# Kernel optimization log

Measured on AMD Instinct MI355X. Metric: run time of the kernel, lower is better.

## Reference

```python
import jax, jax.numpy as jnp
import numpy as np

B, I, H, R = 8192, 512, 1024, 64  # batch, input_size, hidden_size, rank (w_rank == u_ranks[-1])


def setup_inputs() -> dict:
    key = jax.random.key(0)
    ks = jax.random.split(key, 11)
    f = jax.random.normal
    return {
        "x": f(ks[0], (B, I), jnp.float32),
        "h": f(ks[1], (B, H), jnp.float32),
        "c": f(ks[2], (B, H), jnp.float32),
        "u_x": 0.1 * f(ks[3], (I, R), jnp.float32),
        "u_h": 0.1 * f(ks[4], (H, R), jnp.float32),
        "v_x": 0.1 * f(ks[5], (4 * H, R), jnp.float32),
        "v_h": 0.1 * f(ks[6], (4 * H, R), jnp.float32),
        "b_x": 0.1 * f(ks[7], (4 * H,), jnp.float32),
        "b_h": 0.1 * f(ks[8], (4 * H,), jnp.float32),
        "dia_x": 0.1 * f(ks[9], (1, I), jnp.float32),
        "dia_h": 0.1 * f(ks[10], (1, H), jnp.float32),
    }


def reference(x, h, c, u_x, u_h, v_x, v_h, b_x, b_h, dia_x, dia_h):
    Bn = x.shape[0]
    # diagonal (vector-multiplication) terms; vm_x padded to hidden size (H >= I)
    vm_x = jnp.pad(dia_x * x, ((0, 0), (0, H - I)))          # [B, H]
    vm_h = dia_h * h                                          # [B, H]
    # low-rank projections: [B,R] @ [R,4H]
    lowered_x = (x @ u_x) @ v_x.T                             # [B, 4H]
    lowered_h = (h @ u_h) @ v_h.T                             # [B, 4H]
    # vectorized form of the 4-gate refinement loop
    v_x4 = v_x.reshape(4, H, R)
    v_h4 = v_h.reshape(4, H, R)
    coef_x = jnp.sum(u_x[None] * v_x4[:, :I, :], axis=-1)    # [4, I]
    coef_h = jnp.sum(u_h[None] * v_h4, axis=-1)              # [4, H]
    ref_x = jnp.pad(x[:, None, :] * coef_x[None], ((0, 0), (0, 0), (0, H - I))).reshape(Bn, 4 * H)
    ref_h = (h[:, None, :] * coef_h[None]).reshape(Bn, 4 * H)
    gx = lowered_x - ref_x + b_x
    gh = lowered_h - ref_h + b_h
    xi, xf, xo, xn = jnp.split(gx, 4, axis=1)
    hi, hf, ho, hn = jnp.split(gh, 4, axis=1)
    z = vm_x + vm_h
    inputgate = jax.nn.sigmoid(xi + hi + z)
    forgetgate = jax.nn.sigmoid(xf + hf + z)
    outputgate = jax.nn.sigmoid(xo + ho + z)
    newgate = jnp.tanh(xn + hn + z)
    c_next = forgetgate * c + inputgate * newgate
    h_next = outputgate * jnp.tanh(c_next)
    return h_next, c_next
```

## Files before the change

kernel.cpp:

```cpp
#include <hip/hip_runtime.h>
#include <hip/hip_bf16.h>

#define B_ 8192
#define I_ 512
#define H_ 1024
#define R_ 64

typedef __bf16 bf16x8 __attribute__((ext_vector_type(8)));
typedef short  s16x8  __attribute__((ext_vector_type(8)));
typedef float  f32x4  __attribute__((ext_vector_type(4)));

static __device__ __forceinline__ short f2bf(float f) {
    union { float f; unsigned u; } v; v.f = f;
    unsigned r = v.u + 0x7fffu + ((v.u >> 16) & 1u);
    return (short)(r >> 16);
}
static __device__ __forceinline__ float frcp_(float x) {
#if __has_builtin(__builtin_amdgcn_rcpf)
    return __builtin_amdgcn_rcpf(x);
#else
    float r; asm("v_rcp_f32 %0, %1" : "=v"(r) : "v"(x)); return r;
#endif
}
static __device__ __forceinline__ float sigmoidf_(float v) {
    return frcp_(1.f + __expf(-v));
}
static __device__ __forceinline__ float tanhf_(float v) {
    return 2.f * frcp_(1.f + __expf(-2.f * v)) - 1.f;
}

__global__ __launch_bounds__(256) void prep_kernel(
    const float* __restrict__ u_x, const float* __restrict__ u_h,
    const float* __restrict__ v_x, const float* __restrict__ v_h,
    short* __restrict__ uxT, short* __restrict__ uhT, short* __restrict__ Vc,
    float* __restrict__ coef_x, float* __restrict__ coef_h)
{
    int t = blockIdx.x * 256 + threadIdx.x;
    if (t < 64 * 512) {
        int k = t >> 6, r = t & 63;
        uxT[r * 512 + k] = f2bf(u_x[t]);
        return;
    }
    t -= 64 * 512;
    if (t < 64 * 1024) {
        int k = t >> 6, r = t & 63;
        uhT[r * 1024 + k] = f2bf(u_h[t]);
        return;
    }
    t -= 64 * 1024;
    if (t < 4096 * 128) {
        int n = t >> 7, q = t & 127;
        Vc[t] = f2bf(q < 64 ? v_x[n * 64 + q] : v_h[n * 64 + (q - 64)]);
        return;
    }
    t -= 4096 * 128;
    if (t < 1536 * 64) {
        const int wid = t >> 6, lane = t & 63;
        const float* U; const float* V; float* C; int j, JN;
        if (wid < 512) { U = u_x; V = v_x; C = coef_x; j = wid;       JN = 512;  }
        else           { U = u_h; V = v_h; C = coef_h; j = wid - 512; JN = 1024; }
        const float uv = U[(size_t)j * 64 + lane];
        float s[4];
#pragma unroll
        for (int g = 0; g < 4; ++g)
            s[g] = uv * V[(size_t)(g * H_ + j) * 64 + lane];
#pragma unroll
        for (int off = 32; off >= 1; off >>= 1)
#pragma unroll
            for (int g = 0; g < 4; ++g)
                s[g] += __shfl_xor(s[g], off, 64);
        if (lane == 0)
#pragma unroll
            for (int g = 0; g < 4; ++g)
                C[g * JN + j] = s[g];
        return;
    }
}

__global__ __launch_bounds__(256) void stage1_kernel(
    const float* __restrict__ x, const float* __restrict__ h,
    const short* __restrict__ uxT, const short* __restrict__ uhT,
    short* __restrict__ P)
{
    __shared__ short At[16 * 136];
    const int w = threadIdx.x >> 6, lane = threadIdx.x & 63;
    const int quad = lane >> 4, lr = lane & 15;
    const int n0 = w * 16;

    const float* X; const short* UT; int K, co;
    if (blockIdx.y == 0) { X = x; UT = uxT; K = I_; co = 0; }
    else                 { X = h; UT = uhT; K = H_; co = 64; }

    const int b0 = blockIdx.x * 16;
    const int srow = threadIdx.x >> 4;
    const int scol = (threadIdx.x & 15) * 8;

    f32x4 acc = {};
    const short* bp = UT + (size_t)(n0 + lr) * K + quad * 8;
    const short* arow = At + lr * 136 + quad * 8;
    const float* srcbase = X + (size_t)(b0 + srow) * K + scol;

    float4 c0 = ((const float4*)(srcbase))[0];
    float4 c1 = ((const float4*)(srcbase))[1];

    for (int k0 = 0; k0 < K; k0 += 128) {
        s16x8 p;
        p[0] = f2bf(c0.x); p[1] = f2bf(c0.y); p[2] = f2bf(c0.z); p[3] = f2bf(c0.w);
        p[4] = f2bf(c1.x); p[5] = f2bf(c1.y); p[6] = f2bf(c1.z); p[7] = f2bf(c1.w);
        __syncthreads();
        *(s16x8*)(At + srow * 136 + scol) = p;
        __syncthreads();
        if (k0 + 128 < K) {
            c0 = ((const float4*)(srcbase + k0 + 128))[0];
            c1 = ((const float4*)(srcbase + k0 + 128))[1];
        }
#pragma unroll
        for (int ks = 0; ks < 4; ++ks) {
            bf16x8 bfrag = *(const bf16x8*)(bp + k0 + ks * 32);
            bf16x8 afrag = *(const bf16x8*)(arow + ks * 32);
            acc = __builtin_amdgcn_mfma_f32_16x16x32_bf16(afrag, bfrag, acc, 0, 0, 0);
        }
    }

#pragma unroll
    for (int r = 0; r < 4; ++r)
        P[(size_t)(b0 + quad * 4 + r) * 128 + co + n0 + lr] = f2bf(acc[r]);
}

__global__ __launch_bounds__(256) void stage2_kernel(
    const short* __restrict__ P, const short* __restrict__ Vc,
    const float* __restrict__ x, const float* __restrict__ h,
    const float* __restrict__ c,
    const float* __restrict__ coef_x, const float* __restrict__ coef_h,
    const float* __restrict__ b_x, const float* __restrict__ b_h,
    const float* __restrict__ dia_x, const float* __restrict__ dia_h,
    float* __restrict__ out)
{
    const int lane = threadIdx.x & 63;
    const int wv   = threadIdx.x >> 6;
    const int quad = lane >> 4, lr = lane & 15;
    const int b0 = blockIdx.x * 64;
    const int j0 = blockIdx.y * 64 + wv * 16;
    const int j = j0 + lr;
    const bool jx = (j < I_);

    bf16x8 bfr[4][4];
#pragma unroll
    for (int g = 0; g < 4; ++g)
#pragma unroll
        for (int ks = 0; ks < 4; ++ks)
            bfr[g][ks] = *(const bf16x8*)(Vc + (size_t)(g * H_ + j0 + lr) * 128 + ks * 32 + quad * 8);

    const float dx = jx ? dia_x[j] : 0.f;
    const float dh = dia_h[j];
    float cx[4], ch[4], bsum[4];
#pragma unroll
    for (int g = 0; g < 4; ++g) {
        cx[g]   = jx ? coef_x[g * I_ + j] : 0.f;
        ch[g]   = coef_h[g * H_ + j];
        bsum[g] = b_x[g * H_ + j] + b_h[g * H_ + j];
    }

    bf16x8 a[4];
#pragma unroll
    for (int ks = 0; ks < 4; ++ks)
        a[ks] = *(const bf16x8*)(P + (size_t)(b0 + lr) * 128 + ks * 32 + quad * 8);
    float xv[4], hv[4], cv[4];
#pragma unroll
    for (int r = 0; r < 4; ++r) {
        const int brow = b0 + quad * 4 + r;
        cv[r] = c[(size_t)brow * H_ + j];
        hv[r] = h[(size_t)brow * H_ + j];
        xv[r] = jx ? x[(size_t)brow * I_ + j] : 0.f;
    }

    for (int mt = 0; mt < 4; ++mt) {
        bf16x8 an[4];
        float xn[4], hn[4], cn2[4];
        if (mt < 3) {
            const int rb = b0 + (mt + 1) * 16;
#pragma unroll
            for (int ks = 0; ks < 4; ++ks)
                an[ks] = *(const bf16x8*)(P + (size_t)(rb + lr) * 128 + ks * 32 + quad * 8);
#pragma unroll
            for (int r = 0; r < 4; ++r) {
                const int brow = rb + quad * 4 + r;
                cn2[r] = c[(size_t)brow * H_ + j];
                hn[r]  = h[(size_t)brow * H_ + j];
                xn[r]  = jx ? x[(size_t)brow * I_ + j] : 0.f;
            }
        }

        f32x4 acc[4] = {};
#pragma unroll
        for (int ks = 0; ks < 4; ++ks)
#pragma unroll
            for (int g = 0; g < 4; ++g)
                acc[g] = __builtin_amdgcn_mfma_f32_16x16x32_bf16(a[ks], bfr[g][ks], acc[g], 0, 0, 0);

#pragma unroll
        for (int r = 0; r < 4; ++r) {
            const int brow = b0 + mt * 16 + quad * 4 + r;
            const float xe = xv[r], he = hv[r];
            const float z  = dx * xe + dh * he;

            const float g0 = acc[0][r] - xe * cx[0] - he * ch[0] + bsum[0] + z;
            const float g1 = acc[1][r] - xe * cx[1] - he * ch[1] + bsum[1] + z;
            const float g2 = acc[2][r] - xe * cx[2] - he * ch[2] + bsum[2] + z;
            const float g3 = acc[3][r] - xe * cx[3] - he * ch[3] + bsum[3] + z;

            const float ig = sigmoidf_(g0);
            const float fg = sigmoidf_(g1);
            const float og = sigmoidf_(g2);
            const float ng = tanhf_(g3);

            const float cn = fg * cv[r] + ig * ng;
            const float hnv = og * tanhf_(cn);

            out[(size_t)brow * H_ + j] = hnv;
            out[(size_t)B_ * H_ + (size_t)brow * H_ + j] = cn;
        }

        if (mt < 3) {
#pragma unroll
            for (int ks = 0; ks < 4; ++ks) a[ks] = an[ks];
#pragma unroll
            for (int r = 0; r < 4; ++r) { xv[r] = xn[r]; hv[r] = hn[r]; cv[r] = cn2[r]; }
        }
    }
}

extern "C" void kernel_launch(void* const* d_in, const int* in_sizes, int n_in,
                              void* d_out, int out_size, void* d_ws, size_t ws_size,
                              hipStream_t stream) {
    const float* x     = (const float*)d_in[0];
    const float* h     = (const float*)d_in[1];
    const float* c     = (const float*)d_in[2];
    const float* u_x   = (const float*)d_in[3];
    const float* u_h   = (const float*)d_in[4];
    const float* v_x   = (const float*)d_in[5];
    const float* v_h   = (const float*)d_in[6];
    const float* b_x   = (const float*)d_in[7];
    const float* b_h   = (const float*)d_in[8];
    const float* dia_x = (const float*)d_in[9];
    const float* dia_h = (const float*)d_in[10];
    float* out = (float*)d_out;

    char* ws = (char*)d_ws;
    short* P      = (short*)(ws);
    short* uxT    = (short*)(ws + 2097152);
    short* uhT    = (short*)(ws + 2097152 + 65536);
    short* Vc     = (short*)(ws + 2097152 + 65536 + 131072);
    float* coef_x = (float*)(ws + 2097152 + 65536 + 131072 + 1048576);
    float* coef_h = (float*)(ws + 2097152 + 65536 + 131072 + 1048576 + 8192);

    prep_kernel<<<2816, 256, 0, stream>>>(u_x, u_h, v_x, v_h, uxT, uhT, Vc, coef_x, coef_h);
    stage1_kernel<<<dim3(512, 2), 256, 0, stream>>>(x, h, uxT, uhT, P);
    stage2_kernel<<<dim3(128, 16), 256, 0, stream>>>(P, Vc, x, h, c,
                                                     coef_x, coef_h, b_x, b_h,
                                                     dia_x, dia_h, out);
}
```

Before: 194.8 us.

## Swap MFMA operands so each lane owns 4 contiguous hidden columns for vector I/O

The MFMA operand order in stage2 is swapped (V fragment as A, P as B), so the output tile is transposed and each lane holds four consecutive hidden columns of one batch row. This allows 16-byte vector loads of x/h/c and the per-column parameters, and 16-byte nontemporal stores of h_next and c_next, replacing scalar strided accesses. It raises register use for the per-lane 4x4 parameter arrays, and the jx check now uses the warp's column base j0, which relies on I being a multiple of 16.

```diff
diff --git a/kernel.cpp b/kernel.cpp
--- a/kernel.cpp
+++ b/kernel.cpp
@@ -141,91 +141,98 @@
     const int quad = lane >> 4, lr = lane & 15;
     const int b0 = blockIdx.x * 64;
     const int j0 = blockIdx.y * 64 + wv * 16;
-    const int j = j0 + lr;
-    const bool jx = (j < I_);
-
-    bf16x8 bfr[4][4];
-#pragma unroll
-    for (int g = 0; g < 4; ++g)
-#pragma unroll
-        for (int ks = 0; ks < 4; ++ks)
-            bfr[g][ks] = *(const bf16x8*)(Vc + (size_t)(g * H_ + j0 + lr) * 128 + ks * 32 + quad * 8);
-
-    const float dx = jx ? dia_x[j] : 0.f;
-    const float dh = dia_h[j];
-    float cx[4], ch[4], bsum[4];
-#pragma unroll
-    for (int g = 0; g < 4; ++g) {
-        cx[g]   = jx ? coef_x[g * I_ + j] : 0.f;
-        ch[g]   = coef_h[g * H_ + j];
-        bsum[g] = b_x[g * H_ + j] + b_h[g * H_ + j];
-    }
+    const int j4 = j0 + quad * 4;
+    const bool jx = (j0 < I_);
 
     bf16x8 a[4];
 #pragma unroll
     for (int ks = 0; ks < 4; ++ks)
         a[ks] = *(const bf16x8*)(P + (size_t)(b0 + lr) * 128 + ks * 32 + quad * 8);
-    float xv[4], hv[4], cv[4];
-#pragma unroll
-    for (int r = 0; r < 4; ++r) {
-        const int brow = b0 + quad * 4 + r;
-        cv[r] = c[(size_t)brow * H_ + j];
-        hv[r] = h[(size_t)brow * H_ + j];
-        xv[r] = jx ? x[(size_t)brow * I_ + j] : 0.f;
+    f32x4 xv = {}, hv, cv;
+    {
+        const int brow = b0 + lr;
+        cv = *(const f32x4*)(c + (size_t)brow * H_ + j4);
+        hv = *(const f32x4*)(h + (size_t)brow * H_ + j4);
+        if (jx) xv = *(const f32x4*)(x + (size_t)brow * I_ + j4);
+    }
+
+    bf16x8 vfr[4][4];
+#pragma unroll
+    for (int g = 0; g < 4; ++g)
+#pragma unroll
+        for (int ks = 0; ks < 4; ++ks)
+            vfr[g][ks] = *(const bf16x8*)(Vc + (size_t)(g * H_ + j0 + lr) * 128 + ks * 32 + quad * 8);
+
+    float dx[4] = {}, dh[4], cx[4][4] = {}, ch[4][4], bs[4][4];
+    {
+        f32x4 t;
+        if (jx) { t = *(const f32x4*)(dia_x + j4); dx[0]=t[0]; dx[1]=t[1]; dx[2]=t[2]; dx[3]=t[3]; }
+        t = *(const f32x4*)(dia_h + j4); dh[0]=t[0]; dh[1]=t[1]; dh[2]=t[2]; dh[3]=t[3];
+#pragma unroll
+        for (int g = 0; g < 4; ++g) {
+            if (jx) {
+                t = *(const f32x4*)(coef_x + g * I_ + j4);
+                cx[g][0]=t[0]; cx[g][1]=t[1]; cx[g][2]=t[2]; cx[g][3]=t[3];
+            }
+            t = *(const f32x4*)(coef_h + g * H_ + j4);
+            ch[g][0]=t[0]; ch[g][1]=t[1]; ch[g][2]=t[2]; ch[g][3]=t[3];
+            f32x4 tb = *(const f32x4*)(b_x + g * H_ + j4);
+            f32x4 th = *(const f32x4*)(b_h + g * H_ + j4);
+            bs[g][0]=tb[0]+th[0]; bs[g][1]=tb[1]+th[1]; bs[g][2]=tb[2]+th[2]; bs[g][3]=tb[3]+th[3];
+        }
     }
 
     for (int mt = 0; mt < 4; ++mt) {
         bf16x8 an[4];
-        float xn[4], hn[4], cn2[4];
+        f32x4 xn = {}, hn, cn2;
         if (mt < 3) {
-            const int rb = b0 + (mt + 1) * 16;
+            const int rb = b0 + (mt + 1) * 16 + lr;
 #pragma unroll
             for (int ks = 0; ks < 4; ++ks)
-                an[ks] = *(const bf16x8*)(P + (size_t)(rb + lr) * 128 + ks * 32 + quad * 8);
+                an[ks] = *(const bf16x8*)(P + (size_t)rb * 128 + ks * 32 + quad * 8);
+            cn2 = *(const f32x4*)(c + (size_t)rb * H_ + j4);
+            hn  = *(const f32x4*)(h + (size_t)rb * H_ + j4);
+            if (jx) xn = *(const f32x4*)(x + (size_t)rb * I_ + j4);
+        }
+
+        f32x4 acc[4] = {};
+#pragma unroll
+        for (int ks = 0; ks < 4; ++ks)
+#pragma unroll
+            for (int g = 0; g < 4; ++g)
+                acc[g] = __builtin_amdgcn_mfma_f32_16x16x32_bf16(vfr[g][ks], a[ks], acc[g], 0, 0, 0);
+
+        {
+            const int brow = b0 + mt * 16 + lr;
+            float hw[4], cw[4];
 #pragma unroll
             for (int r = 0; r < 4; ++r) {
-                const int brow = rb + quad * 4 + r;
-                cn2[r] = c[(size_t)brow * H_ + j];
-                hn[r]  = h[(size_t)brow * H_ + j];
-                xn[r]  = jx ? x[(size_t)brow * I_ + j] : 0.f;
+                const float xe = xv[r], he = hv[r];
+                const float z  = dx[r] * xe + dh[r] * he;
+
+                const float g0 = acc[0][r] - xe * cx[0][r] - he * ch[0][r] + bs[0][r] + z;
+                const float g1 = acc[1][r] - xe * cx[1][r] - he * ch[1][r] + bs[1][r] + z;
+                const float g2 = acc[2][r] - xe * cx[2][r] - he * ch[2][r] + bs[2][r] + z;
+                const float g3 = acc[3][r] - xe * cx[3][r] - he * ch[3][r] + bs[3][r] + z;
+
+                const float ig = sigmoidf_(g0);
+                const float fg = sigmoidf_(g1);
+                const float og = sigmoidf_(g2);
+                const float ng = tanhf_(g3);
+
+                cw[r] = fg * cv[r] + ig * ng;
+                hw[r] = og * tanhf_(cw[r]);
             }
-        }
-
-        f32x4 acc[4] = {};
-#pragma unroll
-        for (int ks = 0; ks < 4; ++ks)
-#pragma unroll
-            for (int g = 0; g < 4; ++g)
-                acc[g] = __builtin_amdgcn_mfma_f32_16x16x32_bf16(a[ks], bfr[g][ks], acc[g], 0, 0, 0);
-
-#pragma unroll
-        for (int r = 0; r < 4; ++r) {
-            const int brow = b0 + mt * 16 + quad * 4 + r;
-            const float xe = xv[r], he = hv[r];
-            const float z  = dx * xe + dh * he;
-
-            const float g0 = acc[0][r] - xe * cx[0] - he * ch[0] + bsum[0] + z;
-            const float g1 = acc[1][r] - xe * cx[1] - he * ch[1] + bsum[1] + z;
-            const float g2 = acc[2][r] - xe * cx[2] - he * ch[2] + bsum[2] + z;
-            const float g3 = acc[3][r] - xe * cx[3] - he * ch[3] + bsum[3] + z;
-
-            const float ig = sigmoidf_(g0);
-            const float fg = sigmoidf_(g1);
-            const float og = sigmoidf_(g2);
-            const float ng = tanhf_(g3);
-
-            const float cn = fg * cv[r] + ig * ng;
-            const float hnv = og * tanhf_(cn);
-
-            out[(size_t)brow * H_ + j] = hnv;
-            out[(size_t)B_ * H_ + (size_t)brow * H_ + j] = cn;
+            f32x4 hq = { hw[0], hw[1], hw[2], hw[3] };
+            f32x4 cq = { cw[0], cw[1], cw[2], cw[3] };
+            __builtin_nontemporal_store(hq, (f32x4*)(out + (size_t)brow * H_ + j4));
+            __builtin_nontemporal_store(cq, (f32x4*)(out + (size_t)B_ * H_ + (size_t)brow * H_ + j4));
         }
 
         if (mt < 3) {
 #pragma unroll
             for (int ks = 0; ks < 4; ++ks) a[ks] = an[ks];
-#pragma unroll
-            for (int r = 0; r < 4; ++r) { xv[r] = xn[r]; hv[r] = hn[r]; cv[r] = cn2[r]; }
+            xv = xn; hv = hn; cv = cn2;
         }
     }
 }
```

Result: slower. 213.2 us (+9.5%).
